# Kernel optimization log

Measured on AMD Instinct MI355X. Metric: run time of the kernel, lower is better.

## Reference

```python
import jax, jax.numpy as jnp
import numpy as np

N_SEGMENTS = 50000  # number of destination nodes (index values in [0, N_SEGMENTS))


def setup_inputs() -> dict:
    key = jax.random.key(0)
    k1, k2 = jax.random.split(key)
    input = jax.random.normal(k1, (1600000, 64), dtype=jnp.float32)
    index = jax.random.randint(k2, (1600000,), 0, N_SEGMENTS, dtype=jnp.int64)
    return {"input": input, "index": index}


def reference(input, index):
    # Sum-aggregate rows of `input` grouped by `index`: out[n] = sum_{e: index[e]==n} input[e]
    # Equivalent to the custom loma_sum_aggr forward (scatter-add segmented reduction).
    return jax.ops.segment_sum(input, index, num_segments=N_SEGMENTS)
```

## Files before the change

kernel.cpp:

```cpp
#include <hip/hip_runtime.h>
#include <hip/hip_bf16.h>

#define N_SEGMENTS 50000
#define N_ROWS     1600000
#define N_FEAT     64

__global__ void seg_sum_atomic(const float* __restrict__ in,
                               const int*   __restrict__ idx,
                               float*       __restrict__ out) {
    long long t   = (long long)blockIdx.x * blockDim.x + threadIdx.x;
    long long row = t >> 6;
    int       c   = (int)(t & 63);
    if (row < (long long)N_ROWS) {
        int s = idx[row];
        float v = in[row * N_FEAT + c];
        atomicAdd(out + (long long)s * N_FEAT + c, v);
    }
}

extern "C" void kernel_launch(void* const* d_in, const int* in_sizes, int n_in,
                              void* d_out, int out_size, void* d_ws, size_t ws_size,
                              hipStream_t stream) {
    const float* in  = (const float*)d_in[0];
    const int*   idx = (const int*)d_in[1];
    float*       out = (float*)d_out;

    hipMemsetAsync(d_out, 0, (size_t)out_size * sizeof(float), stream);

    const long long total = (long long)N_ROWS * N_FEAT;
    const int block = 256;
    const long long grid = (total + block - 1) / block;

    seg_sum_atomic<<<(unsigned)grid, block, 0, stream>>>(in, idx, out);
}
```

Measured before the change: 737.7 us.

## Replace float atomic scatter with counting-sort CSR build and per-segment wave reduction

Replaces the per-element float atomicAdd scatter with a four-stage pipeline: an integer histogram of segment ids, a single-block exclusive scan to get segment offsets, a scatter of row ids into CSR order, and a reduce kernel in which one wave gathers and sums that segment's rows per feature lane. This removes 102M contended float atomics and the output memset, trading them for integer atomics on the index array plus a random gather of input rows. The single-block scan is serial across 49 chunks and adds launch overhead. Summation order becomes deterministic per segment but differs from the original atomic order.

```diff
diff --git a/kernel.cpp b/kernel.cpp
--- a/kernel.cpp
+++ b/kernel.cpp
@@ -1,21 +1,94 @@
 #include <hip/hip_runtime.h>
-#include <hip/hip_bf16.h>
 
 #define N_SEGMENTS 50000
 #define N_ROWS     1600000
 #define N_FEAT     64
 
-__global__ void seg_sum_atomic(const float* __restrict__ in,
-                               const int*   __restrict__ idx,
-                               float*       __restrict__ out) {
-    long long t   = (long long)blockIdx.x * blockDim.x + threadIdx.x;
-    long long row = t >> 6;
-    int       c   = (int)(t & 63);
-    if (row < (long long)N_ROWS) {
-        int s = idx[row];
-        float v = in[row * N_FEAT + c];
-        atomicAdd(out + (long long)s * N_FEAT + c, v);
+__global__ void hist_kernel(const int* __restrict__ idx, int* __restrict__ counts) {
+    int i = blockIdx.x * 256 + threadIdx.x;
+    if (i < N_ROWS) atomicAdd(&counts[idx[i]], 1);
+}
+
+__device__ __forceinline__ int wave_incl_scan(int v) {
+    int lane = threadIdx.x & 63;
+#pragma unroll
+    for (int d = 1; d < 64; d <<= 1) {
+        int t = __shfl_up(v, d, 64);
+        if (lane >= d) v += t;
     }
+    return v;
+}
+
+__global__ void scan_kernel(const int* __restrict__ counts,
+                            int* __restrict__ seg_start,
+                            int* __restrict__ cursor) {
+    __shared__ int wave_off[16];
+    __shared__ int s_carry;
+    const int tid  = threadIdx.x;
+    const int lane = tid & 63;
+    const int wid  = tid >> 6;
+    if (tid == 0) s_carry = 0;
+    __syncthreads();
+
+    for (int base = 0; base < N_SEGMENTS; base += 1024) {
+        int i = base + tid;
+        int v = (i < N_SEGMENTS) ? counts[i] : 0;
+        int incl = wave_incl_scan(v);
+        if (lane == 63) wave_off[wid] = incl;
+        __syncthreads();
+        if (wid == 0) {
+            int ws    = (lane < 16) ? wave_off[lane] : 0;
+            int wincl = wave_incl_scan(ws);
+            if (lane < 16) wave_off[lane] = wincl - ws;
+        }
+        __syncthreads();
+        int excl = incl - v + wave_off[wid] + s_carry;
+        if (i < N_SEGMENTS) { seg_start[i] = excl; cursor[i] = excl; }
+        __syncthreads();
+        if (tid == 1023) s_carry = excl + v;
+        __syncthreads();
+    }
+    if (tid == 0) seg_start[N_SEGMENTS] = s_carry;
+}
+
+__global__ void scatter_kernel(const int* __restrict__ idx,
+                               int* __restrict__ cursor,
+                               int* __restrict__ rowids) {
+    int i = blockIdx.x * 256 + threadIdx.x;
+    if (i < N_ROWS) {
+        int s = idx[i];
+        int p = atomicAdd(&cursor[s], 1);
+        rowids[p] = i;
+    }
+}
+
+__global__ void __launch_bounds__(256)
+reduce_kernel(const float* __restrict__ in,
+              const int*   __restrict__ rowids,
+              const int*   __restrict__ seg_start,
+              float*       __restrict__ out) {
+    const int wid  = threadIdx.x >> 6;
+    const int lane = threadIdx.x & 63;
+    const int seg  = blockIdx.x * 4 + wid;
+    if (seg >= N_SEGMENTS) return;
+
+    const int beg = seg_start[seg];
+    const int end = seg_start[seg + 1];
+
+    float acc = 0.f;
+    int r = beg;
+    for (; r + 4 <= end; r += 4) {
+        int r0 = rowids[r], r1 = rowids[r + 1], r2 = rowids[r + 2], r3 = rowids[r + 3];
+        float v0 = in[(long long)r0 * N_FEAT + lane];
+        float v1 = in[(long long)r1 * N_FEAT + lane];
+        float v2 = in[(long long)r2 * N_FEAT + lane];
+        float v3 = in[(long long)r3 * N_FEAT + lane];
+        acc += v0; acc += v1; acc += v2; acc += v3;
+    }
+    for (; r < end; ++r)
+        acc += in[(long long)rowids[r] * N_FEAT + lane];
+
+    out[(long long)seg * N_FEAT + lane] = acc;
 }
 
 extern "C" void kernel_launch(void* const* d_in, const int* in_sizes, int n_in,
@@ -25,11 +98,18 @@
     const int*   idx = (const int*)d_in[1];
     float*       out = (float*)d_out;
 
-    hipMemsetAsync(d_out, 0, (size_t)out_size * sizeof(float), stream);
+    int* counts    = (int*)d_ws;
+    int* seg_start = counts + 50048;
+    int* cursor    = seg_start + 50048;
+    int* rowids    = cursor + 50048;
 
-    const long long total = (long long)N_ROWS * N_FEAT;
-    const int block = 256;
-    const long long grid = (total + block - 1) / block;
+    hipMemsetAsync(counts, 0, N_SEGMENTS * sizeof(int), stream);
 
-    seg_sum_atomic<<<(unsigned)grid, block, 0, stream>>>(in, idx, out);
+    const int ROW_BLOCKS = (N_ROWS + 255) / 256;
+    hist_kernel   <<<ROW_BLOCKS, 256, 0, stream>>>(idx, counts);
+    scan_kernel   <<<1, 1024, 0, stream>>>(counts, seg_start, cursor);
+    scatter_kernel<<<ROW_BLOCKS, 256, 0, stream>>>(idx, cursor, rowids);
+
+    const int SEG_BLOCKS = (N_SEGMENTS + 3) / 4;
+    reduce_kernel <<<SEG_BLOCKS, 256, 0, stream>>>(in, rowids, seg_start, out);
 }
```

Result: slower. 786.1 us (+6.6%).
